# Kernel optimization log

Measured on AMD Instinct MI355X. Metric: run time of the kernel, lower is better.

Reference implementation:

```python
import jax, jax.numpy as jnp
import numpy as np

N_NODES = 100000
N_EDGES = 1600000
H = 64
N_LAYERS = 3
NUM_APPS = max(1, N_LAYERS - 1)  # forward applies layer once, then while l>1 loop


def setup_inputs() -> dict:
    key = jax.random.key(0)
    k1, k2, k3, k4, k5 = jax.random.split(key, 5)
    features = jax.random.normal(k1, (N_NODES, H), dtype=jnp.float32)
    W = jax.random.normal(k2, (H, H), dtype=jnp.float32) / np.sqrt(H)
    b = jax.random.normal(k3, (H,), dtype=jnp.float32) * 0.01
    src = jax.random.randint(k4, (N_EDGES,), 0, N_NODES, dtype=jnp.int64)
    dst = jax.random.randint(k5, (N_EDGES,), 0, N_NODES, dtype=jnp.int64)
    return {"features": features, "W": W, "b": b, "src": src, "dst": dst}


def reference(features, W, b, src, dst):
    n = features.shape[0]
    ones = jnp.ones(src.shape[0], dtype=features.dtype)
    # DGL GraphConv norm='both': symmetric normalization, degrees clamped >= 1
    deg_out = jax.ops.segment_sum(ones, src, num_segments=n)
    deg_in = jax.ops.segment_sum(ones, dst, num_segments=n)
    inv_sqrt_out = jnp.clip(deg_out, 1.0, None) ** -0.5  # [N]
    inv_sqrt_in = jnp.clip(deg_in, 1.0, None) ** -0.5    # [N]

    h = features
    for _ in range(NUM_APPS):  # shared-weight GraphConv + ReLU, applied n_layers-1 times
        msg = (h * inv_sqrt_out[:, None])[src]                   # [E, H] gather
        agg = jax.ops.segment_sum(msg, dst, num_segments=n)      # [N, H] scatter-add
        h = jax.nn.relu((agg * inv_sqrt_in[:, None]) @ W + b)    # [N, H]
    return h
```

## Files before the change

kernel.cpp:

```cpp
#include <hip/hip_runtime.h>
#include <hip/hip_fp16.h>

#define N_NODES 100000
#define N_EDGES 1600000
#define HDIM 64
#define NPB 512
#define NPB_SHIFT 9
#define NBUCK 196
#define CAP 16384
#define NCHUNK 256
#define CHUNK (N_EDGES / NCHUNK)

typedef float f4v __attribute__((ext_vector_type(4)));

__global__ void init_kernel(int* __restrict__ gcurD, int* __restrict__ gcurS) {
    int t = threadIdx.x;
    if (t < NBUCK) {
        gcurD[t] = t * CAP;
        gcurS[t] = t * CAP;
    }
}

__device__ inline uint2 f4_to_h4(float x, float y, float z, float w) {
    __half2 lo = __floats2half2_rn(x, y);
    __half2 hi = __floats2half2_rn(z, w);
    uint2 r;
    r.x = *(unsigned*)&lo;
    r.y = *(unsigned*)&hi;
    return r;
}

__global__ void place_kernel(const int* __restrict__ src, const int* __restrict__ dst,
                             int* __restrict__ gcurD, int* __restrict__ gcurS,
                             unsigned int* __restrict__ bufD, unsigned short* __restrict__ bufS) {
    __shared__ int hD[NBUCK], hS[NBUCK], curD[NBUCK], curS[NBUCK];
    int t = threadIdx.x, blk = blockIdx.x;
    for (int i = t; i < NBUCK; i += 256) { hD[i] = 0; hS[i] = 0; }
    __syncthreads();
    int e0 = blk * CHUNK;
    for (int i = t; i < CHUNK; i += 256) {
        atomicAdd(&hD[dst[e0 + i] >> NPB_SHIFT], 1);
        atomicAdd(&hS[src[e0 + i] >> NPB_SHIFT], 1);
    }
    __syncthreads();
    for (int i = t; i < NBUCK; i += 256) {
        curD[i] = hD[i] ? atomicAdd(&gcurD[i], hD[i]) : 0;
        curS[i] = hS[i] ? atomicAdd(&gcurS[i], hS[i]) : 0;
    }
    __syncthreads();
    for (int i = t; i < CHUNK; i += 256) {
        int s = src[e0 + i], d = dst[e0 + i];
        int pd = atomicAdd(&curD[d >> NPB_SHIFT], 1);
        bufD[pd] = (unsigned)s | ((unsigned)(d & (NPB - 1)) << 17);
        int ps = atomicAdd(&curS[s >> NPB_SHIFT], 1);
        bufS[ps] = (unsigned short)(s & (NPB - 1));
    }
}

__global__ void bucket_kernel(const unsigned int* __restrict__ bufD,
                              const unsigned short* __restrict__ bufS,
                              const int* __restrict__ gcurD, const int* __restrict__ gcurS,
                              int* __restrict__ csr_src, int2* __restrict__ offs,
                              float* __restrict__ inv_in, float* __restrict__ inv_out) {
    __shared__ int cnt[NPB], pre[NPB], cur[NPB];
    int t = threadIdx.x;
    int blk = blockIdx.x;
    if (blk < NBUCK) {
        int b = blk;
        int ebase = b * CAP;
        int ecnt  = gcurD[b] - ebase;
        cnt[t] = 0;
        __syncthreads();
        for (int i = t; i < ecnt; i += NPB)
            atomicAdd(&cnt[(int)(bufD[ebase + i] >> 17)], 1);
        __syncthreads();
        int v = cnt[t];
        pre[t] = v;
        __syncthreads();
        for (int off = 1; off < NPB; off <<= 1) {
            int x = (t >= off) ? pre[t - off] : 0;
            __syncthreads(); pre[t] += x; __syncthreads();
        }
        int excl = pre[t] - v;
        cur[t] = excl;
        int node = b * NPB + t;
        if (node < N_NODES) {
            offs[node] = make_int2(ebase + excl, ebase + excl + v);
            inv_in[node] = rsqrtf((float)max(v, 1));
        }
        __syncthreads();
        for (int i = t; i < ecnt; i += NPB) {
            unsigned en = bufD[ebase + i];
            int pos = atomicAdd(&cur[(int)(en >> 17)], 1);
            csr_src[ebase + pos] = (int)(en & 0x1FFFFu);
        }
    } else {
        int b = blk - NBUCK;
        int ebase = b * CAP;
        int ecnt  = gcurS[b] - ebase;
        cnt[t] = 0;
        __syncthreads();
        for (int i = t; i < ecnt; i += NPB)
            atomicAdd(&cnt[(int)bufS[ebase + i]], 1);
        __syncthreads();
        int node = b * NPB + t;
        if (node < N_NODES) inv_out[node] = rsqrtf((float)max(cnt[t], 1));
    }
}

__global__ void dense_kernel(const float* __restrict__ h, const float* __restrict__ inv_out,
                             const float* __restrict__ W, uint2* __restrict__ hw, int n) {
    __shared__ float Wlds[HDIM * HDIM];
    __shared__ float Alds[32][HDIM + 1];
    int t = threadIdx.x;
    int r0 = blockIdx.x * 32;

    for (int i = t; i < HDIM * HDIM / 4; i += 256)
        ((f4v*)Wlds)[i] = ((const f4v*)W)[i];

    for (int i = t; i < 512; i += 256) {
        int r = i >> 4;
        int c4 = i & 15;
        int row = r0 + r;
        f4v v = {0.f, 0.f, 0.f, 0.f};
        float s = 0.f;
        if (row < n) {
            v = __builtin_nontemporal_load((const f4v*)h + (long long)row * 16 + c4);
            s = inv_out[row];
        }
        Alds[r][c4 * 4 + 0] = v.x * s;
        Alds[r][c4 * 4 + 1] = v.y * s;
        Alds[r][c4 * 4 + 2] = v.z * s;
        Alds[r][c4 * 4 + 3] = v.w * s;
    }
    __syncthreads();

    int tx = t & 15;
    int ty = t >> 4;
    float4 acc0 = make_float4(0.f, 0.f, 0.f, 0.f);
    float4 acc1 = acc0;

#pragma unroll 8
    for (int k = 0; k < HDIM; ++k) {
        f4v w = ((const f4v*)(Wlds + k * HDIM))[tx];
        float a0 = Alds[2 * ty + 0][k];
        float a1 = Alds[2 * ty + 1][k];
        acc0.x = fmaf(a0, w.x, acc0.x); acc0.y = fmaf(a0, w.y, acc0.y);
        acc0.z = fmaf(a0, w.z, acc0.z); acc0.w = fmaf(a0, w.w, acc0.w);
        acc1.x = fmaf(a1, w.x, acc1.x); acc1.y = fmaf(a1, w.y, acc1.y);
        acc1.z = fmaf(a1, w.z, acc1.z); acc1.w = fmaf(a1, w.w, acc1.w);
    }

    int rb = r0 + 2 * ty;
    if (rb + 0 < n) hw[(long long)(rb + 0) * 16 + tx] = f4_to_h4(acc0.x, acc0.y, acc0.z, acc0.w);
    if (rb + 1 < n) hw[(long long)(rb + 1) * 16 + tx] = f4_to_h4(acc1.x, acc1.y, acc1.z, acc1.w);
}

__global__ void gather_dense_kernel(const uint4* __restrict__ hw_in, const float* __restrict__ inv_in,
                                    const float* __restrict__ inv_out,
                                    const int2* __restrict__ offs, const int* __restrict__ csr_src,
                                    const float* __restrict__ bias, const float* __restrict__ W,
                                    uint2* __restrict__ hw_out, int n) {
    __shared__ float Wlds[HDIM * HDIM];
    int t = threadIdx.x;
    for (int i = t; i < HDIM * HDIM / 4; i += 256)
        ((f4v*)Wlds)[i] = ((const f4v*)W)[i];

    int wave = t >> 6, lane = t & 63;
    int g = lane >> 3, gl = lane & 7;
    int row = blockIdx.x * 32 + wave * 8 + g;

    float acc0 = 0.f, acc1 = 0.f, acc2 = 0.f, acc3 = 0.f;
    float acc4 = 0.f, acc5 = 0.f, acc6 = 0.f, acc7 = 0.f;

    int2 oe = offs[row];
    int start = oe.x, end = oe.y;
    int gbase = g << 3;

    int jb = start;
    int mm = end - jb; if (mm > 8) mm = 8;
    int sidx = (mm > 0 && gl < mm) ? csr_src[jb + gl] : 0;

    while (jb < end) {
        int jb2 = jb + 8;
        int mm2 = end - jb2; if (mm2 > 8) mm2 = 8;
        int sidx2 = (jb2 < end && gl < mm2) ? csr_src[jb2 + gl] : 0;

        if (mm == 8) {
#pragma unroll
            for (int j = 0; j < 8; ++j) {
                int s = __shfl(sidx, gbase + j, 64);
                uint4 u = hw_in[(long long)s * 8 + gl];
                float2 f0 = __half22float2(*(__half2*)&u.x);
                float2 f1 = __half22float2(*(__half2*)&u.y);
                float2 f2 = __half22float2(*(__half2*)&u.z);
                float2 f3 = __half22float2(*(__half2*)&u.w);
                acc0 += f0.x; acc1 += f0.y; acc2 += f1.x; acc3 += f1.y;
                acc4 += f2.x; acc5 += f2.y; acc6 += f3.x; acc7 += f3.y;
            }
        } else {
            for (int j = 0; j < mm; ++j) {
                int s = __shfl(sidx, gbase + j, 64);
                uint4 u = hw_in[(long long)s * 8 + gl];
                float2 f0 = __half22float2(*(__half2*)&u.x);
                float2 f1 = __half22float2(*(__half2*)&u.y);
                float2 f2 = __half22float2(*(__half2*)&u.z);
                float2 f3 = __half22float2(*(__half2*)&u.w);
                acc0 += f0.x; acc1 += f0.y; acc2 += f1.x; acc3 += f1.y;
                acc4 += f2.x; acc5 += f2.y; acc6 += f3.x; acc7 += f3.y;
            }
        }
        jb = jb2; mm = mm2; sidx = sidx2;
    }

    float sc = inv_in[row];
    float so = inv_out[row];
    float4 b0 = ((const float4*)bias)[gl * 2 + 0];
    float4 b1 = ((const float4*)bias)[gl * 2 + 1];
    f4v h0, h1;
    h0.x = fmaxf(fmaf(acc0, sc, b0.x), 0.f) * so;
    h0.y = fmaxf(fmaf(acc1, sc, b0.y), 0.f) * so;
    h0.z = fmaxf(fmaf(acc2, sc, b0.z), 0.f) * so;
    h0.w = fmaxf(fmaf(acc3, sc, b0.w), 0.f) * so;
    h1.x = fmaxf(fmaf(acc4, sc, b1.x), 0.f) * so;
    h1.y = fmaxf(fmaf(acc5, sc, b1.y), 0.f) * so;
    h1.z = fmaxf(fmaf(acc6, sc, b1.z), 0.f) * so;
    h1.w = fmaxf(fmaf(acc7, sc, b1.w), 0.f) * so;

    __syncthreads();

    float d0 = 0.f, d1 = 0.f, d2 = 0.f, d3 = 0.f;
    float d4 = 0.f, d5 = 0.f, d6 = 0.f, d7 = 0.f;
#pragma unroll
    for (int k = 0; k < HDIM; ++k) {
        float av = ((k >> 2) & 1) ? h1[k & 3] : h0[k & 3];
        float ak = __shfl(av, gbase + (k >> 3), 64);
        f4v w0 = ((const f4v*)Wlds)[k * 16 + gl * 2 + 0];
        f4v w1 = ((const f4v*)Wlds)[k * 16 + gl * 2 + 1];
        d0 = fmaf(ak, w0.x, d0); d1 = fmaf(ak, w0.y, d1);
        d2 = fmaf(ak, w0.z, d2); d3 = fmaf(ak, w0.w, d3);
        d4 = fmaf(ak, w1.x, d4); d5 = fmaf(ak, w1.y, d5);
        d6 = fmaf(ak, w1.z, d6); d7 = fmaf(ak, w1.w, d7);
    }

    hw_out[(long long)row * 16 + gl * 2 + 0] = f4_to_h4(d0, d1, d2, d3);
    hw_out[(long long)row * 16 + gl * 2 + 1] = f4_to_h4(d4, d5, d6, d7);
}

__global__ void gather_kernel(const uint4* __restrict__ hw, const float* __restrict__ inv_in,
                              const int2* __restrict__ offs, const int* __restrict__ csr_src,
                              const float* __restrict__ bias, float* __restrict__ out, int n) {
    int t = threadIdx.x;
    int wave = t >> 6, lane = t & 63;
    int g = lane >> 3, gl = lane & 7;
    int row = blockIdx.x * 32 + wave * 8 + g;
    if (row >= n) return;

    float acc0 = 0.f, acc1 = 0.f, acc2 = 0.f, acc3 = 0.f;
    float acc4 = 0.f, acc5 = 0.f, acc6 = 0.f, acc7 = 0.f;

    int2 oe = offs[row];
    int start = oe.x, end = oe.y;
    int gbase = g << 3;

    int jb = start;
    int mm = end - jb; if (mm > 8) mm = 8;
    int sidx = (mm > 0 && gl < mm) ? csr_src[jb + gl] : 0;

    while (jb < end) {
        int jb2 = jb + 8;
        int mm2 = end - jb2; if (mm2 > 8) mm2 = 8;
        int sidx2 = (jb2 < end && gl < mm2) ? csr_src[jb2 + gl] : 0;

        if (mm == 8) {
#pragma unroll
            for (int j = 0; j < 8; ++j) {
                int s = __shfl(sidx, gbase + j, 64);
                uint4 u = hw[(long long)s * 8 + gl];
                float2 f0 = __half22float2(*(__half2*)&u.x);
                float2 f1 = __half22float2(*(__half2*)&u.y);
                float2 f2 = __half22float2(*(__half2*)&u.z);
                float2 f3 = __half22float2(*(__half2*)&u.w);
                acc0 += f0.x; acc1 += f0.y; acc2 += f1.x; acc3 += f1.y;
                acc4 += f2.x; acc5 += f2.y; acc6 += f3.x; acc7 += f3.y;
            }
        } else {
            for (int j = 0; j < mm; ++j) {
                int s = __shfl(sidx, gbase + j, 64);
                uint4 u = hw[(long long)s * 8 + gl];
                float2 f0 = __half22float2(*(__half2*)&u.x);
                float2 f1 = __half22float2(*(__half2*)&u.y);
                float2 f2 = __half22float2(*(__half2*)&u.z);
                float2 f3 = __half22float2(*(__half2*)&u.w);
                acc0 += f0.x; acc1 += f0.y; acc2 += f1.x; acc3 += f1.y;
                acc4 += f2.x; acc5 += f2.y; acc6 += f3.x; acc7 += f3.y;
            }
        }
        jb = jb2; mm = mm2; sidx = sidx2;
    }

    float sc = inv_in[row];
    float4 b0 = ((const float4*)bias)[gl * 2 + 0];
    float4 b1 = ((const float4*)bias)[gl * 2 + 1];
    f4v r0, r1;
    r0.x = fmaxf(fmaf(acc0, sc, b0.x), 0.f);
    r0.y = fmaxf(fmaf(acc1, sc, b0.y), 0.f);
    r0.z = fmaxf(fmaf(acc2, sc, b0.z), 0.f);
    r0.w = fmaxf(fmaf(acc3, sc, b0.w), 0.f);
    r1.x = fmaxf(fmaf(acc4, sc, b1.x), 0.f);
    r1.y = fmaxf(fmaf(acc5, sc, b1.y), 0.f);
    r1.z = fmaxf(fmaf(acc6, sc, b1.z), 0.f);
    r1.w = fmaxf(fmaf(acc7, sc, b1.w), 0.f);
    __builtin_nontemporal_store(r0, (f4v*)out + (long long)row * 16 + gl * 2 + 0);
    __builtin_nontemporal_store(r1, (f4v*)out + (long long)row * 16 + gl * 2 + 1);
}

extern "C" void kernel_launch(void* const* d_in, const int* in_sizes, int n_in,
                              void* d_out, int out_size, void* d_ws, size_t ws_size,
                              hipStream_t stream) {
    const float* features = (const float*)d_in[0];
    const float* W        = (const float*)d_in[1];
    const float* b        = (const float*)d_in[2];
    const int*   src      = (const int*)d_in[3];
    const int*   dst      = (const int*)d_in[4];

    float* out = (float*)d_out;

    float* ws = (float*)d_ws;
    uint2* hw  = (uint2*)ws;
    uint2* hw2 = (uint2*)(ws + (size_t)N_NODES * 32);
    unsigned int*   bufD = (unsigned int*)(ws + (size_t)N_NODES * 64);
    unsigned short* bufS = (unsigned short*)(bufD + (size_t)NBUCK * CAP);
    int*   csr_src = (int*)(bufS + (size_t)NBUCK * CAP);
    int2*  offs    = (int2*)(csr_src + (size_t)NBUCK * CAP);
    float* inv_out = (float*)(offs + N_NODES);
    float* inv_in  = inv_out + N_NODES;
    int*   gcurD   = (int*)(inv_in + N_NODES);
    int*   gcurS   = gcurD + NBUCK;

    const int N = N_NODES;
    int dense_blocks  = (N + 31) / 32;
    int gather_blocks = (N + 31) / 32;

    init_kernel<<<1, 256, 0, stream>>>(gcurD, gcurS);

    place_kernel<<<NCHUNK, 256, 0, stream>>>(src, dst, gcurD, gcurS, bufD, bufS);

    bucket_kernel<<<2 * NBUCK, NPB, 0, stream>>>(bufD, bufS, gcurD, gcurS,
                                                 csr_src, offs, inv_in, inv_out);

    dense_kernel<<<dense_blocks, 256, 0, stream>>>(features, inv_out, W, hw, N);

    gather_dense_kernel<<<gather_blocks, 256, 0, stream>>>(
        (const uint4*)hw, inv_in, inv_out, offs, csr_src, b, W, hw2, N);

    gather_kernel<<<gather_blocks, 256, 0, stream>>>(
        (const uint4*)hw2, inv_in, offs, csr_src, b, out, N);
}
```

Before: 229.9 us.

## Split final gather into four feature-quarter planes for cache-resident gathers

The second-layer hidden state is now written as four separate 16-feature planes (3.2 MB each) instead of one interleaved array, and the final gather runs as four block groups, each gathering from one plane. The goal is for each plane to fit in L2 so random source-row gathers hit cache rather than HBM. The cost is re-reading the CSR indices four times, which is why those index loads are made nontemporal. The placement chunk count also rises from 256 to 1000.

Measured after the change: 286.7 us. +24.7%, slower.

```diff
diff --git a/kernel.cpp b/kernel.cpp
--- a/kernel.cpp
+++ b/kernel.cpp
@@ -8,10 +8,12 @@
 #define NPB_SHIFT 9
 #define NBUCK 196
 #define CAP 16384
-#define NCHUNK 256
+#define NCHUNK 1000
 #define CHUNK (N_EDGES / NCHUNK)
+#define GBLK 3125
 
 typedef float f4v __attribute__((ext_vector_type(4)));
+typedef float f2v __attribute__((ext_vector_type(2)));
 
 __global__ void init_kernel(int* __restrict__ gcurD, int* __restrict__ gcurS) {
     int t = threadIdx.x;
@@ -160,7 +162,7 @@
                                     const float* __restrict__ inv_out,
                                     const int2* __restrict__ offs, const int* __restrict__ csr_src,
                                     const float* __restrict__ bias, const float* __restrict__ W,
-                                    uint2* __restrict__ hw_out, int n) {
+                                    unsigned* __restrict__ hw2d, int n) {
     __shared__ float Wlds[HDIM * HDIM];
     int t = threadIdx.x;
     for (int i = t; i < HDIM * HDIM / 4; i += 256)
@@ -179,12 +181,12 @@
 
     int jb = start;
     int mm = end - jb; if (mm > 8) mm = 8;
-    int sidx = (mm > 0 && gl < mm) ? csr_src[jb + gl] : 0;
+    int sidx = (mm > 0 && gl < mm) ? __builtin_nontemporal_load(csr_src + jb + gl) : 0;
 
     while (jb < end) {
         int jb2 = jb + 8;
         int mm2 = end - jb2; if (mm2 > 8) mm2 = 8;
-        int sidx2 = (jb2 < end && gl < mm2) ? csr_src[jb2 + gl] : 0;
+        int sidx2 = (jb2 < end && gl < mm2) ? __builtin_nontemporal_load(csr_src + jb2 + gl) : 0;
 
         if (mm == 8) {
 #pragma unroll
@@ -243,76 +245,64 @@
         d6 = fmaf(ak, w1.z, d6); d7 = fmaf(ak, w1.w, d7);
     }
 
-    hw_out[(long long)row * 16 + gl * 2 + 0] = f4_to_h4(d0, d1, d2, d3);
-    hw_out[(long long)row * 16 + gl * 2 + 1] = f4_to_h4(d4, d5, d6, d7);
-}
-
-__global__ void gather_kernel(const uint4* __restrict__ hw, const float* __restrict__ inv_in,
-                              const int2* __restrict__ offs, const int* __restrict__ csr_src,
-                              const float* __restrict__ bias, float* __restrict__ out, int n) {
+    uint2 p01 = f4_to_h4(d0, d1, d2, d3);
+    uint2 p23 = f4_to_h4(d4, d5, d6, d7);
+    uint4 pack = make_uint4(p01.x, p01.y, p23.x, p23.y);
+    *(uint4*)(hw2d + (((size_t)(gl >> 1) * N_NODES + row) * 8) + (gl & 1) * 4) = pack;
+}
+
+__global__ void gather_q_kernel(const unsigned* __restrict__ hw2d, const float* __restrict__ inv_in,
+                                const int2* __restrict__ offs, const int* __restrict__ csr_src,
+                                const float* __restrict__ bias, float* __restrict__ out, int n) {
+    int bid = blockIdx.x;
+    int q  = bid / GBLK;
+    int rb = bid - q * GBLK;
     int t = threadIdx.x;
     int wave = t >> 6, lane = t & 63;
     int g = lane >> 3, gl = lane & 7;
-    int row = blockIdx.x * 32 + wave * 8 + g;
+    int row = rb * 32 + wave * 8 + g;
     if (row >= n) return;
-
-    float acc0 = 0.f, acc1 = 0.f, acc2 = 0.f, acc3 = 0.f;
-    float acc4 = 0.f, acc5 = 0.f, acc6 = 0.f, acc7 = 0.f;
+    const unsigned* plane = hw2d + (size_t)q * N_NODES * 8;
+
+    float acc0 = 0.f, acc1 = 0.f;
 
     int2 oe = offs[row];
-    int start = oe.x, end = oe.y;
+    int jb = oe.x, end = oe.y;
     int gbase = g << 3;
 
-    int jb = start;
     int mm = end - jb; if (mm > 8) mm = 8;
-    int sidx = (mm > 0 && gl < mm) ? csr_src[jb + gl] : 0;
+    int sidx = (mm > 0 && gl < mm) ? __builtin_nontemporal_load(csr_src + jb + gl) : 0;
 
     while (jb < end) {
         int jb2 = jb + 8;
         int mm2 = end - jb2; if (mm2 > 8) mm2 = 8;
-        int sidx2 = (jb2 < end && gl < mm2) ? csr_src[jb2 + gl] : 0;
+        int sidx2 = (jb2 < end && gl < mm2) ? __builtin_nontemporal_load(csr_src + jb2 + gl) : 0;
 
         if (mm == 8) {
 #pragma unroll
             for (int j = 0; j < 8; ++j) {
                 int s = __shfl(sidx, gbase + j, 64);
-                uint4 u = hw[(long long)s * 8 + gl];
-                float2 f0 = __half22float2(*(__half2*)&u.x);
-                float2 f1 = __half22float2(*(__half2*)&u.y);
-                float2 f2 = __half22float2(*(__half2*)&u.z);
-                float2 f3 = __half22float2(*(__half2*)&u.w);
-                acc0 += f0.x; acc1 += f0.y; acc2 += f1.x; acc3 += f1.y;
-                acc4 += f2.x; acc5 += f2.y; acc6 += f3.x; acc7 += f3.y;
+                unsigned u = plane[s * 8 + gl];
+                float2 f = __half22float2(*(__half2*)&u);
+                acc0 += f.x; acc1 += f.y;
             }
         } else {
             for (int j = 0; j < mm; ++j) {
                 int s = __shfl(sidx, gbase + j, 64);
-                uint4 u = hw[(long long)s * 8 + gl];
-                float2 f0 = __half22float2(*(__half2*)&u.x);
-                float2 f1 = __half22float2(*(__half2*)&u.y);
-                float2 f2 = __half22float2(*(__half2*)&u.z);
-                float2 f3 = __half22float2(*(__half2*)&u.w);
-                acc0 += f0.x; acc1 += f0.y; acc2 += f1.x; acc3 += f1.y;
-                acc4 += f2.x; acc5 += f2.y; acc6 += f3.x; acc7 += f3.y;
+                unsigned u = plane[s * 8 + gl];
+                float2 f = __half22float2(*(__half2*)&u);
+                acc0 += f.x; acc1 += f.y;
             }
         }
         jb = jb2; mm = mm2; sidx = sidx2;
     }
 
     float sc = inv_in[row];
-    float4 b0 = ((const float4*)bias)[gl * 2 + 0];
-    float4 b1 = ((const float4*)bias)[gl * 2 + 1];
-    f4v r0, r1;
-    r0.x = fmaxf(fmaf(acc0, sc, b0.x), 0.f);
-    r0.y = fmaxf(fmaf(acc1, sc, b0.y), 0.f);
-    r0.z = fmaxf(fmaf(acc2, sc, b0.z), 0.f);
-    r0.w = fmaxf(fmaf(acc3, sc, b0.w), 0.f);
-    r1.x = fmaxf(fmaf(acc4, sc, b1.x), 0.f);
-    r1.y = fmaxf(fmaf(acc5, sc, b1.y), 0.f);
-    r1.z = fmaxf(fmaf(acc6, sc, b1.z), 0.f);
-    r1.w = fmaxf(fmaf(acc7, sc, b1.w), 0.f);
-    __builtin_nontemporal_store(r0, (f4v*)out + (long long)row * 16 + gl * 2 + 0);
-    __builtin_nontemporal_store(r1, (f4v*)out + (long long)row * 16 + gl * 2 + 1);
+    f2v bb = ((const f2v*)bias)[q * 8 + gl];
+    f2v r;
+    r.x = fmaxf(fmaf(acc0, sc, bb.x), 0.f);
+    r.y = fmaxf(fmaf(acc1, sc, bb.y), 0.f);
+    __builtin_nontemporal_store(r, (f2v*)out + (size_t)row * 32 + q * 8 + gl);
 }
 
 extern "C" void kernel_launch(void* const* d_in, const int* in_sizes, int n_in,
@@ -327,8 +317,8 @@
     float* out = (float*)d_out;
 
     float* ws = (float*)d_ws;
-    uint2* hw  = (uint2*)ws;
-    uint2* hw2 = (uint2*)(ws + (size_t)N_NODES * 32);
+    uint2*    hw   = (uint2*)ws;
+    unsigned* hw2d = (unsigned*)(ws + (size_t)N_NODES * 32);
     unsigned int*   bufD = (unsigned int*)(ws + (size_t)N_NODES * 64);
     unsigned short* bufS = (unsigned short*)(bufD + (size_t)NBUCK * CAP);
     int*   csr_src = (int*)(bufS + (size_t)NBUCK * CAP);
@@ -339,8 +329,6 @@
     int*   gcurS   = gcurD + NBUCK;
 
     const int N = N_NODES;
-    int dense_blocks  = (N + 31) / 32;
-    int gather_blocks = (N + 31) / 32;
 
     init_kernel<<<1, 256, 0, stream>>>(gcurD, gcurS);
 
@@ -349,11 +337,11 @@
     bucket_kernel<<<2 * NBUCK, NPB, 0, stream>>>(bufD, bufS, gcurD, gcurS,
                                                  csr_src, offs, inv_in, inv_out);
 
-    dense_kernel<<<dense_blocks, 256, 0, stream>>>(features, inv_out, W, hw, N);
-
-    gather_dense_kernel<<<gather_blocks, 256, 0, stream>>>(
-        (const uint4*)hw, inv_in, inv_out, offs, csr_src, b, W, hw2, N);
-
-    gather_kernel<<<gather_blocks, 256, 0, stream>>>(
-        (const uint4*)hw2, inv_in, offs, csr_src, b, out, N);
-}
+    dense_kernel<<<GBLK, 256, 0, stream>>>(features, inv_out, W, hw, N);
+
+    gather_dense_kernel<<<GBLK, 256, 0, stream>>>(
+        (const uint4*)hw, inv_in, inv_out, offs, csr_src, b, W, hw2d, N);
+
+    gather_q_kernel<<<4 * GBLK, 256, 0, stream>>>(
+        hw2d, inv_in, offs, csr_src, b, out, N);
+}
```

## Fuse first dense transform into source-degree bucket blocks and use wave-shuffle scan

Applied to the files above, without the earlier changes.

Removes the separate dense_kernel launch. The source-degree bucket blocks now also compute inv_out locally in LDS and immediately run the first 64x64 transform on their 512 rows, writing fp16 output. The per-bucket exclusive prefix scan changes from a barrier-heavy LDS Hillis-Steele loop to wave shuffles plus a small cross-wave sum. The dense work now runs on only 196 large blocks alongside the CSR-building blocks, trading dense-phase parallelism for one fewer launch and no reread of inv_out.

Result: slower. 698.2 us (+203.6%).

```diff
diff --git a/kernel.cpp b/kernel.cpp
--- a/kernel.cpp
+++ b/kernel.cpp
@@ -10,6 +10,7 @@
 #define CAP 16384
 #define NCHUNK 256
 #define CHUNK (N_EDGES / NCHUNK)
+#define GBLK 3125
 
 typedef float f4v __attribute__((ext_vector_type(4)));
 
@@ -57,15 +58,18 @@
     }
 }
 
-__global__ void bucket_kernel(const unsigned int* __restrict__ bufD,
-                              const unsigned short* __restrict__ bufS,
-                              const int* __restrict__ gcurD, const int* __restrict__ gcurS,
-                              int* __restrict__ csr_src, int2* __restrict__ offs,
-                              float* __restrict__ inv_in, float* __restrict__ inv_out) {
-    __shared__ int cnt[NPB], pre[NPB], cur[NPB];
+__global__ void bucket_dense_kernel(const unsigned int* __restrict__ bufD,
+                                    const unsigned short* __restrict__ bufS,
+                                    const int* __restrict__ gcurD, const int* __restrict__ gcurS,
+                                    int* __restrict__ csr_src, int2* __restrict__ offs,
+                                    float* __restrict__ inv_in, float* __restrict__ inv_out,
+                                    const float* __restrict__ h, const float* __restrict__ W,
+                                    uint2* __restrict__ hw, int n) {
     int t = threadIdx.x;
     int blk = blockIdx.x;
     if (blk < NBUCK) {
+        __shared__ int cnt[NPB], cur[NPB];
+        __shared__ int wsum[8];
         int b = blk;
         int ebase = b * CAP;
         int ecnt  = gcurD[b] - ebase;
@@ -75,13 +79,19 @@
             atomicAdd(&cnt[(int)(bufD[ebase + i] >> 17)], 1);
         __syncthreads();
         int v = cnt[t];
-        pre[t] = v;
-        __syncthreads();
-        for (int off = 1; off < NPB; off <<= 1) {
-            int x = (t >= off) ? pre[t - off] : 0;
-            __syncthreads(); pre[t] += x; __syncthreads();
-        }
-        int excl = pre[t] - v;
+        int lane = t & 63, w = t >> 6;
+        int p = v;
+#pragma unroll
+        for (int d = 1; d < 64; d <<= 1) {
+            int x = __shfl_up(p, d, 64);
+            if (lane >= d) p += x;
+        }
+        if (lane == 63) wsum[w] = p;
+        __syncthreads();
+        int base = 0;
+#pragma unroll
+        for (int i = 0; i < 8; ++i) base += (i < w) ? wsum[i] : 0;
+        int excl = base + p - v;
         cur[t] = excl;
         int node = b * NPB + t;
         if (node < N_NODES) {
@@ -95,65 +105,57 @@
             csr_src[ebase + pos] = (int)(en & 0x1FFFFu);
         }
     } else {
+        __shared__ int scnt[NPB];
+        __shared__ float sinv[NPB];
+        __shared__ float Wlds[HDIM * HDIM];
         int b = blk - NBUCK;
         int ebase = b * CAP;
         int ecnt  = gcurS[b] - ebase;
-        cnt[t] = 0;
+        for (int i = t; i < HDIM * HDIM / 4; i += 512)
+            ((f4v*)Wlds)[i] = ((const f4v*)W)[i];
+        scnt[t] = 0;
         __syncthreads();
         for (int i = t; i < ecnt; i += NPB)
-            atomicAdd(&cnt[(int)bufS[ebase + i]], 1);
-        __syncthreads();
+            atomicAdd(&scnt[(int)bufS[ebase + i]], 1);
+        __syncthreads();
+        float inv = rsqrtf((float)max(scnt[t], 1));
         int node = b * NPB + t;
-        if (node < N_NODES) inv_out[node] = rsqrtf((float)max(cnt[t], 1));
-    }
-}
-
-__global__ void dense_kernel(const float* __restrict__ h, const float* __restrict__ inv_out,
-                             const float* __restrict__ W, uint2* __restrict__ hw, int n) {
-    __shared__ float Wlds[HDIM * HDIM];
-    __shared__ float Alds[32][HDIM + 1];
-    int t = threadIdx.x;
-    int r0 = blockIdx.x * 32;
-
-    for (int i = t; i < HDIM * HDIM / 4; i += 256)
-        ((f4v*)Wlds)[i] = ((const f4v*)W)[i];
-
-    for (int i = t; i < 512; i += 256) {
-        int r = i >> 4;
-        int c4 = i & 15;
-        int row = r0 + r;
-        f4v v = {0.f, 0.f, 0.f, 0.f};
-        float s = 0.f;
-        if (row < n) {
-            v = __builtin_nontemporal_load((const f4v*)h + (long long)row * 16 + c4);
-            s = inv_out[row];
-        }
-        Alds[r][c4 * 4 + 0] = v.x * s;
-        Alds[r][c4 * 4 + 1] = v.y * s;
-        Alds[r][c4 * 4 + 2] = v.z * s;
-        Alds[r][c4 * 4 + 3] = v.w * s;
-    }
-    __syncthreads();
-
-    int tx = t & 15;
-    int ty = t >> 4;
-    float4 acc0 = make_float4(0.f, 0.f, 0.f, 0.f);
-    float4 acc1 = acc0;
-
-#pragma unroll 8
-    for (int k = 0; k < HDIM; ++k) {
-        f4v w = ((const f4v*)(Wlds + k * HDIM))[tx];
-        float a0 = Alds[2 * ty + 0][k];
-        float a1 = Alds[2 * ty + 1][k];
-        acc0.x = fmaf(a0, w.x, acc0.x); acc0.y = fmaf(a0, w.y, acc0.y);
-        acc0.z = fmaf(a0, w.z, acc0.z); acc0.w = fmaf(a0, w.w, acc0.w);
-        acc1.x = fmaf(a1, w.x, acc1.x); acc1.y = fmaf(a1, w.y, acc1.y);
-        acc1.z = fmaf(a1, w.z, acc1.z); acc1.w = fmaf(a1, w.w, acc1.w);
-    }
-
-    int rb = r0 + 2 * ty;
-    if (rb + 0 < n) hw[(long long)(rb + 0) * 16 + tx] = f4_to_h4(acc0.x, acc0.y, acc0.z, acc0.w);
-    if (rb + 1 < n) hw[(long long)(rb + 1) * 16 + tx] = f4_to_h4(acc1.x, acc1.y, acc1.z, acc1.w);
+        if (node < n) inv_out[node] = inv;
+        sinv[t] = inv;
+        __syncthreads();
+
+        int rr = t >> 3, gl = t & 7;
+        int gbase = (t & 63) & 56;
+        for (int pss = 0; pss < 8; ++pss) {
+            int r = pss * 64 + rr;
+            int row = b * NPB + r;
+            f4v a0 = {0.f, 0.f, 0.f, 0.f}, a1 = a0;
+            if (row < n) {
+                float so = sinv[r];
+                a0 = __builtin_nontemporal_load((const f4v*)h + (long long)row * 16 + gl * 2 + 0);
+                a1 = __builtin_nontemporal_load((const f4v*)h + (long long)row * 16 + gl * 2 + 1);
+                a0.x *= so; a0.y *= so; a0.z *= so; a0.w *= so;
+                a1.x *= so; a1.y *= so; a1.z *= so; a1.w *= so;
+            }
+            float acc0 = 0.f, acc1 = 0.f, acc2 = 0.f, acc3 = 0.f;
+            float acc4 = 0.f, acc5 = 0.f, acc6 = 0.f, acc7 = 0.f;
+#pragma unroll
+            for (int k = 0; k < HDIM; ++k) {
+                float av = ((k >> 2) & 1) ? a1[k & 3] : a0[k & 3];
+                float ak = __shfl(av, gbase + (k >> 3), 64);
+                f4v w0 = ((const f4v*)Wlds)[k * 16 + gl * 2 + 0];
+                f4v w1 = ((const f4v*)Wlds)[k * 16 + gl * 2 + 1];
+                acc0 = fmaf(ak, w0.x, acc0); acc1 = fmaf(ak, w0.y, acc1);
+                acc2 = fmaf(ak, w0.z, acc2); acc3 = fmaf(ak, w0.w, acc3);
+                acc4 = fmaf(ak, w1.x, acc4); acc5 = fmaf(ak, w1.y, acc5);
+                acc6 = fmaf(ak, w1.z, acc6); acc7 = fmaf(ak, w1.w, acc7);
+            }
+            if (row < n) {
+                hw[(long long)row * 16 + gl * 2 + 0] = f4_to_h4(acc0, acc1, acc2, acc3);
+                hw[(long long)row * 16 + gl * 2 + 1] = f4_to_h4(acc4, acc5, acc6, acc7);
+            }
+        }
+    }
 }
 
 __global__ void gather_dense_kernel(const uint4* __restrict__ hw_in, const float* __restrict__ inv_in,
@@ -260,10 +262,9 @@
     float acc4 = 0.f, acc5 = 0.f, acc6 = 0.f, acc7 = 0.f;
 
     int2 oe = offs[row];
-    int start = oe.x, end = oe.y;
+    int jb = oe.x, end = oe.y;
     int gbase = g << 3;
 
-    int jb = start;
     int mm = end - jb; if (mm > 8) mm = 8;
     int sidx = (mm > 0 && gl < mm) ? csr_src[jb + gl] : 0;
 
@@ -339,21 +340,18 @@
     int*   gcurS   = gcurD + NBUCK;
 
     const int N = N_NODES;
-    int dense_blocks  = (N + 31) / 32;
-    int gather_blocks = (N + 31) / 32;
 
     init_kernel<<<1, 256, 0, stream>>>(gcurD, gcurS);
 
     place_kernel<<<NCHUNK, 256, 0, stream>>>(src, dst, gcurD, gcurS, bufD, bufS);
 
-    bucket_kernel<<<2 * NBUCK, NPB, 0, stream>>>(bufD, bufS, gcurD, gcurS,
-                                                 csr_src, offs, inv_in, inv_out);
-
-    dense_kernel<<<dense_blocks, 256, 0, stream>>>(features, inv_out, W, hw, N);
-
-    gather_dense_kernel<<<gather_blocks, 256, 0, stream>>>(
+    bucket_dense_kernel<<<2 * NBUCK, NPB, 0, stream>>>(
+        bufD, bufS, gcurD, gcurS, csr_src, offs, inv_in, inv_out,
+        features, W, hw, N);
+
+    gather_dense_kernel<<<GBLK, 256, 0, stream>>>(
         (const uint4*)hw, inv_in, inv_out, offs, csr_src, b, W, hw2, N);
 
-    gather_kernel<<<gather_blocks, 256, 0, stream>>>(
+    gather_kernel<<<GBLK, 256, 0, stream>>>(
         (const uint4*)hw2, inv_in, offs, csr_src, b, out, N);
 }
```
